# Kernel tuning notes

Measured on AMD Instinct MI355X. Metric: run time of the kernel, lower is better.

The kernel has to match this reference:

```python
import jax, jax.numpy as jnp
import numpy as np

BS, N, HX, HL, HY = 512, 128, 256, 64, 128
EPS = 1e-5  # nn.LayerNorm default


def setup_inputs() -> dict:
    key = jax.random.key(0)
    ks = jax.random.split(key, 10)

    def lin(k, fan_in, fan_out):
        return jax.random.normal(k, (fan_in, fan_out), jnp.float32) / np.float32(np.sqrt(fan_in))

    return {
        "X": jax.random.normal(ks[0], (BS, N, HX), jnp.float32),
        "E": jax.random.randint(ks[1], (BS, N, N, 2), 0, 2, jnp.int32),
        "y": jax.random.normal(ks[2], (BS, HY), jnp.float32),
        "label": jax.random.normal(ks[3], (BS, N, HL), jnp.float32),
        "node_mask": jnp.ones((BS, N), jnp.bool_),
        # GCNConv aggr_X: (HX+HL) -> HX ; GCNConv aggr_label: HL -> HL
        "Wx": lin(ks[4], HX + HL, HX), "bx": jnp.zeros((HX,), jnp.float32),
        "Wl": lin(ks[5], HL, HL), "bl": jnp.zeros((HL,), jnp.float32),
        # update_X: Linear(HX+HL+HY -> HX) + ReLU + LayerNorm
        "W1": lin(ks[6], HX + HL + HY, HX), "b1": jnp.zeros((HX,), jnp.float32),
        "g1": jnp.ones((HX,), jnp.float32), "be1": jnp.zeros((HX,), jnp.float32),
        # update_label: Linear(HL -> HL) + ReLU + LayerNorm
        "W2": lin(ks[7], HL, HL), "b2": jnp.zeros((HL,), jnp.float32),
        "g2": jnp.ones((HL,), jnp.float32), "be2": jnp.zeros((HL,), jnp.float32),
    }


def _layernorm(h, g, b):
    mu = jnp.mean(h, axis=-1, keepdims=True)
    var = jnp.mean((h - mu) ** 2, axis=-1, keepdims=True)
    return (h - mu) * jax.lax.rsqrt(var + EPS) * g + b


def _gcn_norm_adj(E, node_mask, dtype):
    # adj = E[..., 1] nonzero pattern, restricted to valid nodes.
    adj = (E[..., 1] != 0).astype(dtype)  # [bs, n, n]
    m = node_mask.astype(dtype)
    adj = adj * m[:, :, None] * m[:, None, :]
    # GCNConv default: add self-loops, symmetric normalization D^-1/2 (A+I) D^-1/2
    A = adj + jnp.eye(adj.shape[-1], dtype=dtype)[None]
    deg = jnp.sum(A, axis=-1)
    dinv = jnp.where(deg > 0, jax.lax.rsqrt(jnp.maximum(deg, 1.0)), 0.0)
    return A * dinv[:, :, None] * dinv[:, None, :]


def reference(X, E, y, label, node_mask,
              Wx, bx, Wl, bl,
              W1, b1, g1, be1,
              W2, b2, g2, be2):
    bs, n, hx = X.shape
    _, hy = y.shape
    An = _gcn_norm_adj(E, node_mask, X.dtype)  # [bs, n, n]

    # aggr_X: GCNConv on cat([X, label])
    Xl = jnp.concatenate([X, label], axis=-1)              # [bs, n, hx+hl]
    Xa = jnp.einsum('bij,bjh->bih', An, Xl @ Wx) + bx      # [bs, n, hx]
    # aggr_label: GCNConv on label
    la = jnp.einsum('bij,bjh->bih', An, label @ Wl) + bl   # [bs, n, hl]

    y_expand = jnp.broadcast_to(y[:, None, :], (bs, n, hy))
    h = jnp.concatenate([Xa, la, y_expand], axis=-1)       # [bs, n, hx+hl+hy]

    X_out = _layernorm(jax.nn.relu(h @ W1 + b1), g1, be1)  # dropout in eval = identity
    label_out = _layernorm(jax.nn.relu(la @ W2 + b2), g2, be2)
    return (X_out, label_out)
```

## Files before the change

### kernel.cpp

```cpp
#include <hip/hip_runtime.h>


typedef __attribute__((ext_vector_type(8))) short bf16x8;
typedef __attribute__((ext_vector_type(4))) float f32x4;
typedef unsigned short u16;
typedef unsigned int u32;

#define OFF_WXT 0
#define OFF_W1T 81920
#define OFF_WLT 196608
#define OFF_W2T 200704
#define WS_U16  204800

__device__ __forceinline__ u16 f2bf(float f) {
  u32 u = __float_as_uint(f);
  return (u16)((u + 0x7FFFu + ((u >> 16) & 1u)) >> 16);
}
__device__ __forceinline__ float bf2f(u16 h) {
  return __uint_as_float(((u32)h) << 16);
}
__device__ __forceinline__ u32 pk2(float x, float y) {
  return (u32)f2bf(x) | ((u32)f2bf(y) << 16);
}
__device__ __forceinline__ bf16x8 pack8(float4 a, float4 b) {
  union { bf16x8 v; u32 u[4]; } r;
  r.u[0] = pk2(a.x, a.y); r.u[1] = pk2(a.z, a.w);
  r.u[2] = pk2(b.x, b.y); r.u[3] = pk2(b.z, b.w);
  return r.v;
}

#define MFMA(a, bfr, c) __builtin_amdgcn_mfma_f32_16x16x32_bf16((a), (bfr), (c), 0, 0, 0)

__global__ __launch_bounds__(256)
void wprep_kernel(const float* __restrict__ Wx, const float* __restrict__ Wl,
                  const float* __restrict__ W1, const float* __restrict__ W2,
                  u16* __restrict__ ws) {
  int t = blockIdx.x * 256 + threadIdx.x;
  if (t >= WS_U16) return;
  float v;
  if (t < 81920) {
    int n = t / 320, k = t - n * 320;
    v = Wx[k * 256 + n];
  } else if (t < 196608) {
    int t2 = t - 81920;
    int n = t2 / 448, k = t2 - n * 448;
    v = W1[k * 256 + n];
  } else if (t < 200704) {
    int t3 = t - 196608;
    int n = t3 >> 6, k = t3 & 63;
    v = Wl[k * 64 + n];
  } else {
    int t4 = t - 200704;
    int n = t4 >> 6, k = t4 & 63;
    v = W2[k * 64 + n];
  }
  ws[t] = f2bf(v);
}

__global__ __launch_bounds__(1024, 4)
void gnn_fused(const float* __restrict__ Xg, const int* __restrict__ Eg,
               const float* __restrict__ yg, const float* __restrict__ Lb,
               const float* __restrict__ bx, const float* __restrict__ blv,
               const float* __restrict__ b1, const float* __restrict__ g1,
               const float* __restrict__ be1, const float* __restrict__ b2,
               const float* __restrict__ g2, const float* __restrict__ be2,
               const u16* __restrict__ wsW,
               float* __restrict__ Xout, float* __restrict__ Lout) {
  __shared__ u16 sA[128 * 136];
  __shared__ u16 sXWT[256 * 136];
  __shared__ u16 sLWT[64 * 136];
  __shared__ u16 sH[128 * 72];
  __shared__ u16 sXbf[128 * 72];
  __shared__ float sBX[256];
  __shared__ float sBL[64];
  __shared__ float sW1YB[256];
  __shared__ float sDinv[128];
  __shared__ float2 sRed[256];

  const int tid = threadIdx.x;
  const int w = tid >> 6;
  const int lane = tid & 63;
  const int quad = lane >> 4;
  const int l15 = lane & 15;
  const int b = blockIdx.x;

  float* sDegp = reinterpret_cast<float*>(sH);
  float* sY    = reinterpret_cast<float*>(sH) + 1024;

  bf16x8 afx[10];
  {
    const u16* wrow = wsW + OFF_WXT + (w * 16 + l15) * 320 + quad * 8;
    #pragma unroll
    for (int cc = 0; cc < 10; ++cc) afx[cc] = *reinterpret_cast<const bf16x8*>(wrow + cc * 32);
  }
  bf16x8 afl[2];
  {
    const u16* wrow = wsW + OFF_WLT + ((w & 3) * 16 + l15) * 64 + quad * 8;
    afl[0] = *reinterpret_cast<const bf16x8*>(wrow);
    afl[1] = *reinterpret_cast<const bf16x8*>(wrow + 32);
  }

  if (tid < 256) sBX[tid] = bx[tid];
  else if (tid < 320) sBL[tid - 256] = blv[tid - 256];
  else if (tid < 448) sY[tid - 320] = yg[(size_t)b * 128 + (tid - 320)];

  {
    const int i = tid >> 3;
    const int qq = tid & 7;
    const int4* Erow = reinterpret_cast<const int4*>(Eg) + (size_t)b * 8192 + i * 64 + qq * 8;
    float part = 0.f;
    #pragma unroll
    for (int cc = 0; cc < 8; ++cc) {
      int4 v = Erow[cc];
      int j = qq * 16 + cc * 2;
      float a0 = (v.y != 0) ? 1.f : 0.f;
      float a1 = (v.w != 0) ? 1.f : 0.f;
      if (j == i) a0 += 1.f;
      if (j + 1 == i) a1 += 1.f;
      part += a0 + a1;
      *reinterpret_cast<u32*>(&sA[i * 136 + j]) = pk2(a0, a1);
    }
    sDegp[i * 8 + qq] = part;
  }
  __syncthreads();

  if (tid < 128) {
    float d = 0.f;
    #pragma unroll
    for (int k = 0; k < 8; ++k) d += sDegp[tid * 8 + k];
    sDinv[tid] = (d > 0.f) ? rsqrtf(fmaxf(d, 1.f)) : 0.f;
  }
  if (tid < 256) {
    float s = b1[tid];
    const u16* rowp = wsW + OFF_W1T + tid * 448 + 320;
    #pragma unroll
    for (int kk = 0; kk < 128; kk += 8) {
      bf16x8 v = *reinterpret_cast<const bf16x8*>(rowp + kk);
      #pragma unroll
      for (int t2 = 0; t2 < 8; ++t2) s += bf2f((u16)v[t2]) * sY[kk + t2];
    }
    sW1YB[tid] = s;
  }

  f32x4 acc1[8];
  #pragma unroll
  for (int jt = 0; jt < 8; ++jt) acc1[jt] = f32x4{0.f, 0.f, 0.f, 0.f};

  for (int c = 0; c < 5; ++c) {
    __syncthreads();
    {
      int j = tid >> 3;
      int kk = (tid & 7) * 8;
      const float* src = (c < 4) ? (Xg + ((size_t)(b * 128 + j)) * 256 + c * 64 + kk)
                                 : (Lb + ((size_t)(b * 128 + j)) * 64 + kk);
      float4 v0 = *reinterpret_cast<const float4*>(src);
      float4 v1 = *reinterpret_cast<const float4*>(src + 4);
      *reinterpret_cast<bf16x8*>(&sXbf[j * 72 + kk]) = pack8(v0, v1);
    }
    __syncthreads();
    #pragma unroll
    for (int ks = 0; ks < 2; ++ks) {
      #pragma unroll
      for (int jt = 0; jt < 8; ++jt) {
        bf16x8 bfr = *reinterpret_cast<const bf16x8*>(&sXbf[(jt * 16 + l15) * 72 + ks * 32 + quad * 8]);
        acc1[jt] = MFMA(afx[c * 2 + ks], bfr, acc1[jt]);
      }
    }
  }
  f32x4 accl[2];
  accl[0] = f32x4{0.f, 0.f, 0.f, 0.f};
  accl[1] = f32x4{0.f, 0.f, 0.f, 0.f};
  {
    const int jh = w >> 2;
    #pragma unroll
    for (int ks = 0; ks < 2; ++ks) {
      #pragma unroll
      for (int jj = 0; jj < 2; ++jj) {
        int j = (jh * 2 + jj) * 16 + l15;
        bf16x8 bfr = *reinterpret_cast<const bf16x8*>(&sXbf[j * 72 + ks * 32 + quad * 8]);
        accl[jj] = MFMA(afl[ks], bfr, accl[jj]);
      }
    }
  }
  #pragma unroll
  for (int jt = 0; jt < 8; ++jt) {
    float dj = sDinv[jt * 16 + l15];
    #pragma unroll
    for (int r = 0; r < 4; ++r)
      sXWT[(w * 16 + quad * 4 + r) * 136 + jt * 16 + l15] = f2bf(acc1[jt][r] * dj);
  }
  #pragma unroll
  for (int jj = 0; jj < 2; ++jj) {
    int j = ((w >> 2) * 2 + jj) * 16 + l15;
    float dj = sDinv[j];
    #pragma unroll
    for (int r = 0; r < 4; ++r)
      sLWT[((w & 3) * 16 + quad * 4 + r) * 136 + j] = f2bf(accl[jj][r] * dj);
  }
  __syncthreads();

  const int g = w >> 1, p = w & 1;
  const int i_ = g * 16 + l15;
  const float di = sDinv[i_];

  f32x4 acc3[8];
  #pragma unroll
  for (int m = 0; m < 8; ++m) {
    float4 iv = *reinterpret_cast<const float4*>(&sW1YB[(p * 8 + m) * 16 + quad * 4]);
    acc3[m][0] = iv.x; acc3[m][1] = iv.y; acc3[m][2] = iv.z; acc3[m][3] = iv.w;
  }

  for (int c = 0; c < 5; ++c) {
    const u16* Ablk = (c < 4) ? (sXWT + (c * 64) * 136) : sLWT;
    f32x4 acc2[2];
    acc2[0] = f32x4{0.f, 0.f, 0.f, 0.f};
    acc2[1] = f32x4{0.f, 0.f, 0.f, 0.f};
    #pragma unroll
    for (int ks = 0; ks < 4; ++ks) {
      bf16x8 bfr = *reinterpret_cast<const bf16x8*>(&sA[i_ * 136 + ks * 32 + quad * 8]);
      #pragma unroll
      for (int mtl = 0; mtl < 2; ++mtl) {
        bf16x8 af = *reinterpret_cast<const bf16x8*>(Ablk + ((p * 2 + mtl) * 16 + l15) * 136 + ks * 32 + quad * 8);
        acc2[mtl] = MFMA(af, bfr, acc2[mtl]);
      }
    }
    if (c > 0) __syncthreads();
    #pragma unroll
    for (int mtl = 0; mtl < 2; ++mtl) {
      ushort4 pk;
      u16* pp = reinterpret_cast<u16*>(&pk);
      #pragma unroll
      for (int r = 0; r < 4; ++r) {
        int nloc = (p * 2 + mtl) * 16 + quad * 4 + r;
        float bias = (c < 4) ? sBX[c * 64 + nloc] : sBL[nloc];
        pp[r] = f2bf(acc2[mtl][r] * di + bias);
      }
      *reinterpret_cast<ushort4*>(&sH[i_ * 72 + (p * 2 + mtl) * 16 + quad * 4]) = pk;
    }
    __syncthreads();
    #pragma unroll
    for (int ks2 = 0; ks2 < 2; ++ks2) {
      bf16x8 bh = *reinterpret_cast<const bf16x8*>(&sH[i_ * 72 + ks2 * 32 + quad * 8]);
      #pragma unroll
      for (int m = 0; m < 8; ++m) {
        bf16x8 af = *reinterpret_cast<const bf16x8*>(wsW + OFF_W1T + ((p * 8 + m) * 16 + l15) * 448 + c * 64 + ks2 * 32 + quad * 8);
        acc3[m] = MFMA(af, bh, acc3[m]);
      }
    }
  }

  {
    float s = 0.f, s2 = 0.f;
    #pragma unroll
    for (int m = 0; m < 8; ++m) {
      #pragma unroll
      for (int r = 0; r < 4; ++r) {
        float v = fmaxf(acc3[m][r], 0.f);
        acc3[m][r] = v;
        s += v; s2 += v * v;
      }
    }
    s  += __shfl_xor(s, 16);  s  += __shfl_xor(s, 32);
    s2 += __shfl_xor(s2, 16); s2 += __shfl_xor(s2, 32);
    if (quad == 0) sRed[p * 128 + i_] = make_float2(s, s2);
    __syncthreads();
    float2 o = sRed[(1 - p) * 128 + i_];
    s += o.x; s2 += o.y;
    float mu = s * (1.f / 256.f);
    float var = s2 * (1.f / 256.f) - mu * mu;
    float rstd = rsqrtf(var + 1e-5f);
    float* op = Xout + ((size_t)(b * 128 + i_)) * 256;
    #pragma unroll
    for (int m = 0; m < 8; ++m) {
      int f0 = (p * 8 + m) * 16 + quad * 4;
      float4 gv = *reinterpret_cast<const float4*>(g1 + f0);
      float4 bv = *reinterpret_cast<const float4*>(be1 + f0);
      float4 o4;
      o4.x = (acc3[m][0] - mu) * rstd * gv.x + bv.x;
      o4.y = (acc3[m][1] - mu) * rstd * gv.y + bv.y;
      o4.z = (acc3[m][2] - mu) * rstd * gv.z + bv.z;
      o4.w = (acc3[m][3] - mu) * rstd * gv.w + bv.w;
      *reinterpret_cast<float4*>(op + f0) = o4;
    }
  }

  if (p == 0) {
    f32x4 acc4[4];
    #pragma unroll
    for (int mt2 = 0; mt2 < 4; ++mt2) acc4[mt2] = f32x4{0.f, 0.f, 0.f, 0.f};
    #pragma unroll
    for (int ks = 0; ks < 2; ++ks) {
      bf16x8 bh = *reinterpret_cast<const bf16x8*>(&sH[i_ * 72 + ks * 32 + quad * 8]);
      #pragma unroll
      for (int mt2 = 0; mt2 < 4; ++mt2) {
        bf16x8 af = *reinterpret_cast<const bf16x8*>(wsW + OFF_W2T + (mt2 * 16 + l15) * 64 + ks * 32 + quad * 8);
        acc4[mt2] = MFMA(af, bh, acc4[mt2]);
      }
    }
    float s = 0.f, s2 = 0.f;
    #pragma unroll
    for (int mt2 = 0; mt2 < 4; ++mt2) {
      float4 bias2 = *reinterpret_cast<const float4*>(b2 + mt2 * 16 + quad * 4);
      acc4[mt2][0] = fmaxf(acc4[mt2][0] + bias2.x, 0.f);
      acc4[mt2][1] = fmaxf(acc4[mt2][1] + bias2.y, 0.f);
      acc4[mt2][2] = fmaxf(acc4[mt2][2] + bias2.z, 0.f);
      acc4[mt2][3] = fmaxf(acc4[mt2][3] + bias2.w, 0.f);
      #pragma unroll
      for (int r = 0; r < 4; ++r) { s += acc4[mt2][r]; s2 += acc4[mt2][r] * acc4[mt2][r]; }
    }
    s  += __shfl_xor(s, 16);  s  += __shfl_xor(s, 32);
    s2 += __shfl_xor(s2, 16); s2 += __shfl_xor(s2, 32);
    float mu = s * (1.f / 64.f);
    float var = s2 * (1.f / 64.f) - mu * mu;
    float rstd = rsqrtf(var + 1e-5f);
    float* op = Lout + ((size_t)(b * 128 + i_)) * 64;
    #pragma unroll
    for (int mt2 = 0; mt2 < 4; ++mt2) {
      int f0 = mt2 * 16 + quad * 4;
      float4 gv = *reinterpret_cast<const float4*>(g2 + f0);
      float4 bv = *reinterpret_cast<const float4*>(be2 + f0);
      float4 o4;
      o4.x = (acc4[mt2][0] - mu) * rstd * gv.x + bv.x;
      o4.y = (acc4[mt2][1] - mu) * rstd * gv.y + bv.y;
      o4.z = (acc4[mt2][2] - mu) * rstd * gv.z + bv.z;
      o4.w = (acc4[mt2][3] - mu) * rstd * gv.w + bv.w;
      *reinterpret_cast<float4*>(op + f0) = o4;
    }
  }
}

extern "C" void kernel_launch(void* const* d_in, const int* in_sizes, int n_in,
                              void* d_out, int out_size, void* d_ws, size_t ws_size,
                              hipStream_t stream) {
  (void)in_sizes; (void)n_in; (void)out_size; (void)ws_size;
  const float* X   = (const float*)d_in[0];
  const int*   E   = (const int*)d_in[1];
  const float* y   = (const float*)d_in[2];
  const float* lb  = (const float*)d_in[3];
  const float* Wx  = (const float*)d_in[5];
  const float* bx  = (const float*)d_in[6];
  const float* Wl  = (const float*)d_in[7];
  const float* bl  = (const float*)d_in[8];
  const float* W1  = (const float*)d_in[9];
  const float* b1  = (const float*)d_in[10];
  const float* g1  = (const float*)d_in[11];
  const float* be1 = (const float*)d_in[12];
  const float* W2  = (const float*)d_in[13];
  const float* b2  = (const float*)d_in[14];
  const float* g2  = (const float*)d_in[15];
  const float* be2 = (const float*)d_in[16];
  u16* wsW = (u16*)d_ws;
  float* Xout = (float*)d_out;
  float* Lout = Xout + (size_t)512 * 128 * 256;

  wprep_kernel<<<dim3(800), dim3(256), 0, stream>>>(Wx, Wl, W1, W2, wsW);
  gnn_fused<<<dim3(512), dim3(1024), 0, stream>>>(X, E, y, lb, bx, bl, b1, g1, be1,
                                                  b2, g2, be2, wsW, Xout, Lout);
}
```

Before: 333.2 us.

## Shrink LDS by streaming XW chunks through one buffer and reloading weights per chunk

Replaces the full sXWT/sLWT staging buffers with a single 64-row chunk buffer that each wave group fills just before it is consumed, and aliases the bf16 X staging onto sH. Wx/Wl fragments are now loaded from global memory per chunk instead of held in registers for the whole kernel, and the launch bound asks for higher occupancy. The aim is to cut LDS and register use so more blocks fit per CU. In exchange it adds a barrier per chunk, keeps the projection results in registers across phases, and issues more global weight loads.

```diff
diff --git a/kernel.cpp b/kernel.cpp
--- a/kernel.cpp
+++ b/kernel.cpp
@@ -57,7 +57,7 @@
   ws[t] = f2bf(v);
 }
 
-__global__ __launch_bounds__(1024, 4)
+__global__ __launch_bounds__(1024, 8)
 void gnn_fused(const float* __restrict__ Xg, const int* __restrict__ Eg,
                const float* __restrict__ yg, const float* __restrict__ Lb,
                const float* __restrict__ bx, const float* __restrict__ blv,
@@ -67,10 +67,8 @@
                const u16* __restrict__ wsW,
                float* __restrict__ Xout, float* __restrict__ Lout) {
   __shared__ u16 sA[128 * 136];
-  __shared__ u16 sXWT[256 * 136];
-  __shared__ u16 sLWT[64 * 136];
+  __shared__ u16 sChunk[64 * 136];
   __shared__ u16 sH[128 * 72];
-  __shared__ u16 sXbf[128 * 72];
   __shared__ float sBX[256];
   __shared__ float sBL[64];
   __shared__ float sW1YB[256];
@@ -84,21 +82,9 @@
   const int l15 = lane & 15;
   const int b = blockIdx.x;
 
+  u16* sXbf = sH;
   float* sDegp = reinterpret_cast<float*>(sH);
   float* sY    = reinterpret_cast<float*>(sH) + 1024;
-
-  bf16x8 afx[10];
-  {
-    const u16* wrow = wsW + OFF_WXT + (w * 16 + l15) * 320 + quad * 8;
-    #pragma unroll
-    for (int cc = 0; cc < 10; ++cc) afx[cc] = *reinterpret_cast<const bf16x8*>(wrow + cc * 32);
-  }
-  bf16x8 afl[2];
-  {
-    const u16* wrow = wsW + OFF_WLT + ((w & 3) * 16 + l15) * 64 + quad * 8;
-    afl[0] = *reinterpret_cast<const bf16x8*>(wrow);
-    afl[1] = *reinterpret_cast<const bf16x8*>(wrow + 32);
-  }
 
   if (tid < 256) sBX[tid] = bx[tid];
   else if (tid < 320) sBL[tid - 256] = blv[tid - 256];
@@ -157,46 +143,78 @@
       float4 v1 = *reinterpret_cast<const float4*>(src + 4);
       *reinterpret_cast<bf16x8*>(&sXbf[j * 72 + kk]) = pack8(v0, v1);
     }
-    __syncthreads();
-    #pragma unroll
-    for (int ks = 0; ks < 2; ++ks) {
-      #pragma unroll
-      for (int jt = 0; jt < 8; ++jt) {
-        bf16x8 bfr = *reinterpret_cast<const bf16x8*>(&sXbf[(jt * 16 + l15) * 72 + ks * 32 + quad * 8]);
-        acc1[jt] = MFMA(afx[c * 2 + ks], bfr, acc1[jt]);
-      }
+    const u16* wr = wsW + OFF_WXT + (w * 16 + l15) * 320 + c * 64 + quad * 8;
+    bf16x8 af0 = *reinterpret_cast<const bf16x8*>(wr);
+    bf16x8 af1 = *reinterpret_cast<const bf16x8*>(wr + 32);
+    __syncthreads();
+    #pragma unroll
+    for (int jt = 0; jt < 8; ++jt) {
+      bf16x8 bfr = *reinterpret_cast<const bf16x8*>(&sXbf[(jt * 16 + l15) * 72 + quad * 8]);
+      acc1[jt] = MFMA(af0, bfr, acc1[jt]);
+    }
+    #pragma unroll
+    for (int jt = 0; jt < 8; ++jt) {
+      bf16x8 bfr = *reinterpret_cast<const bf16x8*>(&sXbf[(jt * 16 + l15) * 72 + 32 + quad * 8]);
+      acc1[jt] = MFMA(af1, bfr, acc1[jt]);
     }
   }
   f32x4 accl[2];
   accl[0] = f32x4{0.f, 0.f, 0.f, 0.f};
   accl[1] = f32x4{0.f, 0.f, 0.f, 0.f};
   {
+    const u16* wrl = wsW + OFF_WLT + ((w & 3) * 16 + l15) * 64 + quad * 8;
+    bf16x8 al0 = *reinterpret_cast<const bf16x8*>(wrl);
+    bf16x8 al1 = *reinterpret_cast<const bf16x8*>(wrl + 32);
     const int jh = w >> 2;
     #pragma unroll
-    for (int ks = 0; ks < 2; ++ks) {
-      #pragma unroll
-      for (int jj = 0; jj < 2; ++jj) {
-        int j = (jh * 2 + jj) * 16 + l15;
-        bf16x8 bfr = *reinterpret_cast<const bf16x8*>(&sXbf[j * 72 + ks * 32 + quad * 8]);
-        accl[jj] = MFMA(afl[ks], bfr, accl[jj]);
-      }
-    }
-  }
+    for (int jj = 0; jj < 2; ++jj) {
+      int j = (jh * 2 + jj) * 16 + l15;
+      bf16x8 b0 = *reinterpret_cast<const bf16x8*>(&sXbf[j * 72 + quad * 8]);
+      accl[jj] = MFMA(al0, b0, accl[jj]);
+      bf16x8 b1 = *reinterpret_cast<const bf16x8*>(&sXbf[j * 72 + 32 + quad * 8]);
+      accl[jj] = MFMA(al1, b1, accl[jj]);
+    }
+  }
+
+  u32 xpk[16];
   #pragma unroll
   for (int jt = 0; jt < 8; ++jt) {
     float dj = sDinv[jt * 16 + l15];
-    #pragma unroll
-    for (int r = 0; r < 4; ++r)
-      sXWT[(w * 16 + quad * 4 + r) * 136 + jt * 16 + l15] = f2bf(acc1[jt][r] * dj);
-  }
+    xpk[jt * 2]     = pk2(acc1[jt][0] * dj, acc1[jt][1] * dj);
+    xpk[jt * 2 + 1] = pk2(acc1[jt][2] * dj, acc1[jt][3] * dj);
+  }
+  u32 lpk[4];
   #pragma unroll
   for (int jj = 0; jj < 2; ++jj) {
-    int j = ((w >> 2) * 2 + jj) * 16 + l15;
-    float dj = sDinv[j];
-    #pragma unroll
-    for (int r = 0; r < 4; ++r)
-      sLWT[((w & 3) * 16 + quad * 4 + r) * 136 + j] = f2bf(accl[jj][r] * dj);
-  }
+    float dj = sDinv[((w >> 2) * 2 + jj) * 16 + l15];
+    lpk[jj * 2]     = pk2(accl[jj][0] * dj, accl[jj][1] * dj);
+    lpk[jj * 2 + 1] = pk2(accl[jj][2] * dj, accl[jj][3] * dj);
+  }
+
+  auto write_xchunk = [&]() {
+    const int rbase = (w & 3) * 16 + quad * 4;
+    #pragma unroll
+    for (int jt = 0; jt < 8; ++jt) {
+      int j = jt * 16 + l15;
+      sChunk[(rbase + 0) * 136 + j] = (u16)(xpk[jt * 2] & 0xffffu);
+      sChunk[(rbase + 1) * 136 + j] = (u16)(xpk[jt * 2] >> 16);
+      sChunk[(rbase + 2) * 136 + j] = (u16)(xpk[jt * 2 + 1] & 0xffffu);
+      sChunk[(rbase + 3) * 136 + j] = (u16)(xpk[jt * 2 + 1] >> 16);
+    }
+  };
+  auto write_lchunk = [&]() {
+    const int rbase = (w & 3) * 16 + quad * 4;
+    #pragma unroll
+    for (int jj = 0; jj < 2; ++jj) {
+      int j = ((w >> 2) * 2 + jj) * 16 + l15;
+      sChunk[(rbase + 0) * 136 + j] = (u16)(lpk[jj * 2] & 0xffffu);
+      sChunk[(rbase + 1) * 136 + j] = (u16)(lpk[jj * 2] >> 16);
+      sChunk[(rbase + 2) * 136 + j] = (u16)(lpk[jj * 2 + 1] & 0xffffu);
+      sChunk[(rbase + 3) * 136 + j] = (u16)(lpk[jj * 2 + 1] >> 16);
+    }
+  };
+
+  if ((w >> 2) == 0) write_xchunk();
   __syncthreads();
 
   const int g = w >> 1, p = w & 1;
@@ -211,7 +229,6 @@
   }
 
   for (int c = 0; c < 5; ++c) {
-    const u16* Ablk = (c < 4) ? (sXWT + (c * 64) * 136) : sLWT;
     f32x4 acc2[2];
     acc2[0] = f32x4{0.f, 0.f, 0.f, 0.f};
     acc2[1] = f32x4{0.f, 0.f, 0.f, 0.f};
@@ -220,11 +237,11 @@
       bf16x8 bfr = *reinterpret_cast<const bf16x8*>(&sA[i_ * 136 + ks * 32 + quad * 8]);
       #pragma unroll
       for (int mtl = 0; mtl < 2; ++mtl) {
-        bf16x8 af = *reinterpret_cast<const bf16x8*>(Ablk + ((p * 2 + mtl) * 16 + l15) * 136 + ks * 32 + quad * 8);
+        bf16x8 af = *reinterpret_cast<const bf16x8*>(&sChunk[((p * 2 + mtl) * 16 + l15) * 136 + ks * 32 + quad * 8]);
         acc2[mtl] = MFMA(af, bfr, acc2[mtl]);
       }
     }
-    if (c > 0) __syncthreads();
+    __syncthreads();
     #pragma unroll
     for (int mtl = 0; mtl < 2; ++mtl) {
       ushort4 pk;
@@ -236,6 +253,11 @@
         pp[r] = f2bf(acc2[mtl][r] * di + bias);
       }
       *reinterpret_cast<ushort4*>(&sH[i_ * 72 + (p * 2 + mtl) * 16 + quad * 4]) = pk;
+    }
+    if (c < 3) {
+      if ((w >> 2) == c + 1) write_xchunk();
+    } else if (c == 3) {
+      write_lchunk();
     }
     __syncthreads();
     #pragma unroll
```

After: 399.9 us. 20.0% more time.

## Split fused GNN kernel into prep, feature-transform and aggregate+update kernels

Applied to the files above, without the earlier changes.

Replaces the single 1024-thread-per-batch fused kernel with three launches. A prep kernel transposes weights through shared memory, precomputes the per-batch y@W1 contribution plus bias, and builds the bf16 adjacency with self-loops and dinv. A 256-thread kernel computes dinv-scaled X·Wx and label·Wl into workspace. A second kernel splits each batch into four row-groups for aggregation, the W1/W2 linears and both layernorms. This trades extra global traffic through workspace and more launches for many more, smaller blocks and better occupancy. The old fused path is kept as a fallback when the workspace is too small.

```diff
diff --git a/kernel.cpp b/kernel.cpp
--- a/kernel.cpp
+++ b/kernel.cpp
@@ -5,12 +5,17 @@
 typedef __attribute__((ext_vector_type(4))) float f32x4;
 typedef unsigned short u16;
 typedef unsigned int u32;
+typedef unsigned char u8;
 
 #define OFF_WXT 0
 #define OFF_W1T 81920
 #define OFF_WLT 196608
 #define OFF_W2T 200704
-#define WS_U16  204800
+#define OFF_WYB 204800
+#define OFF_AB  466944
+#define OFF_DINV 8855552
+#define OFF_XWT 8986624
+#define WS_NEED 59916288ull
 
 __device__ __forceinline__ u16 f2bf(float f) {
   u32 u = __float_as_uint(f);
@@ -32,29 +37,311 @@
 #define MFMA(a, bfr, c) __builtin_amdgcn_mfma_f32_16x16x32_bf16((a), (bfr), (c), 0, 0, 0)
 
 __global__ __launch_bounds__(256)
-void wprep_kernel(const float* __restrict__ Wx, const float* __restrict__ Wl,
-                  const float* __restrict__ W1, const float* __restrict__ W2,
-                  u16* __restrict__ ws) {
-  int t = blockIdx.x * 256 + threadIdx.x;
-  if (t >= WS_U16) return;
-  float v;
-  if (t < 81920) {
-    int n = t / 320, k = t - n * 320;
-    v = Wx[k * 256 + n];
-  } else if (t < 196608) {
-    int t2 = t - 81920;
-    int n = t2 / 448, k = t2 - n * 448;
-    v = W1[k * 256 + n];
-  } else if (t < 200704) {
-    int t3 = t - 196608;
-    int n = t3 >> 6, k = t3 & 63;
-    v = Wl[k * 64 + n];
+void prep_kernel(const float* __restrict__ Wx, const float* __restrict__ Wl,
+                 const float* __restrict__ W1, const float* __restrict__ W2,
+                 const float* __restrict__ b1, const float* __restrict__ yg,
+                 const int* __restrict__ Eg, u16* __restrict__ ws) {
+  __shared__ __align__(16) u8 smem[34048];
+  const int bid = blockIdx.x;
+  const int tid = threadIdx.x;
+
+  if (bid < 50) {
+    u16 (*tile)[65] = (u16(*)[65])smem;
+    const float* src; u16* dst; int R, C, kt, nt;
+    if (bid < 20)       { src = Wx; dst = ws + OFF_WXT; R = 320; C = 256; kt = bid / 4; nt = bid & 3; }
+    else if (bid < 48)  { src = W1; dst = ws + OFF_W1T; R = 448; C = 256; kt = (bid - 20) / 4; nt = (bid - 20) & 3; }
+    else if (bid == 48) { src = Wl; dst = ws + OFF_WLT; R = 64; C = 64; kt = 0; nt = 0; }
+    else                { src = W2; dst = ws + OFF_W2T; R = 64; C = 64; kt = 0; nt = 0; }
+    const int k0 = kt * 64, n0 = nt * 64;
+    const int tr = tid >> 6, tc = tid & 63;
+    #pragma unroll
+    for (int rr = 0; rr < 16; ++rr)
+      tile[rr * 4 + tr][tc] = f2bf(src[(size_t)(k0 + rr * 4 + tr) * C + n0 + tc]);
+    __syncthreads();
+    #pragma unroll
+    for (int rr = 0; rr < 16; ++rr)
+      dst[(size_t)(n0 + rr * 4 + tr) * R + k0 + tc] = tile[tc][rr * 4 + tr];
+
+  } else if (bid < 562) {
+    float* sY = (float*)smem;
+    const int b = bid - 50, f = tid;
+    if (tid < 128) sY[tid] = yg[(size_t)b * 128 + tid];
+    __syncthreads();
+    float s = b1[f];
+    const float* wcol = W1 + (size_t)320 * 256 + f;
+    #pragma unroll 8
+    for (int d = 0; d < 128; ++d)
+      s += bf2f(f2bf(wcol[(size_t)d * 256])) * sY[d];
+    ((float*)(ws + OFF_WYB))[(size_t)b * 256 + f] = s;
+
   } else {
-    int t4 = t - 200704;
-    int n = t4 >> 6, k = t4 & 63;
-    v = W2[k * 64 + n];
-  }
-  ws[t] = f2bf(v);
+    const int b = bid - 562;
+    u16* sAr = (u16*)smem;
+    const int4* E4 = (const int4*)Eg + (size_t)b * 8192;
+    #pragma unroll
+    for (int t = 0; t < 32; ++t) {
+      int fi = tid + t * 256;
+      int i = fi >> 6, j = (fi & 63) * 2;
+      int4 v = E4[fi];
+      float a0 = (v.y != 0) ? 1.f : 0.f;
+      float a1 = (v.w != 0) ? 1.f : 0.f;
+      if (j == i) a0 += 1.f;
+      if (j + 1 == i) a1 += 1.f;
+      *(u32*)&sAr[i * 132 + j] = pk2(a0, a1);
+    }
+    __syncthreads();
+    if (tid < 128) {
+      float d = 0.f;
+      const u32* row = (const u32*)&sAr[tid * 132];
+      #pragma unroll
+      for (int t = 0; t < 64; ++t) {
+        u32 u = row[t];
+        d += bf2f((u16)(u & 0xffffu)) + bf2f((u16)(u >> 16));
+      }
+      ((float*)(ws + OFF_DINV))[(size_t)b * 128 + tid] =
+          (d > 0.f) ? rsqrtf(fmaxf(d, 1.f)) : 0.f;
+    }
+    u32* dst = (u32*)(ws + OFF_AB) + (size_t)b * 8192;
+    #pragma unroll
+    for (int t = 0; t < 32; ++t) {
+      int o = tid + t * 256;
+      int row = o >> 6, c = o & 63;
+      dst[o] = *(const u32*)&sAr[row * 132 + c * 2];
+    }
+  }
+}
+
+__global__ __launch_bounds__(256)
+void a1_kernel(const float* __restrict__ Xg, const float* __restrict__ Lb,
+               const u16* __restrict__ wsW, const float* __restrict__ dinvg,
+               u16* __restrict__ XWT) {
+  __shared__ u16 sXbf[128 * 72];
+  __shared__ float sDinv[128];
+  int bid = blockIdx.x;
+  bid = (bid & 7) * 320 + (bid >> 3);
+  const int b = bid / 5, fq = bid % 5;
+  const int tid = threadIdx.x;
+  const int wv = tid >> 6, lane = tid & 63, quad = lane >> 4, l15 = lane & 15;
+
+  if (tid < 128) sDinv[tid] = dinvg[(size_t)b * 128 + tid];
+
+  f32x4 acc[8];
+  #pragma unroll
+  for (int jt = 0; jt < 8; ++jt) acc[jt] = f32x4{0.f, 0.f, 0.f, 0.f};
+
+  const int frow0 = (fq < 4 ? fq * 64 : 256) + wv * 16;
+  const u16* wbase = (fq < 4) ? (wsW + OFF_WXT + (size_t)(frow0 + l15) * 320)
+                              : (wsW + OFF_WLT + (size_t)(wv * 16 + l15) * 64);
+  const int c0 = (fq < 4) ? 0 : 4;
+
+  for (int c = c0; c < 5; ++c) {
+    __syncthreads();
+    {
+      int j = tid >> 1, kh = tid & 1;
+      const float* src = (c < 4) ? (Xg + ((size_t)(b * 128 + j)) * 256 + c * 64 + kh * 32)
+                                 : (Lb + ((size_t)(b * 128 + j)) * 64 + kh * 32);
+      #pragma unroll
+      for (int t = 0; t < 2; ++t) {
+        float4 v0 = *(const float4*)(src + t * 16);
+        float4 v1 = *(const float4*)(src + t * 16 + 4);
+        float4 v2 = *(const float4*)(src + t * 16 + 8);
+        float4 v3 = *(const float4*)(src + t * 16 + 12);
+        *(bf16x8*)&sXbf[j * 72 + kh * 32 + t * 16] = pack8(v0, v1);
+        *(bf16x8*)&sXbf[j * 72 + kh * 32 + t * 16 + 8] = pack8(v2, v3);
+      }
+    }
+    const int kc = (fq < 4) ? c * 64 : 0;
+    bf16x8 af0 = *(const bf16x8*)(wbase + kc + quad * 8);
+    bf16x8 af1 = *(const bf16x8*)(wbase + kc + 32 + quad * 8);
+    __syncthreads();
+    #pragma unroll
+    for (int jt = 0; jt < 8; ++jt)
+      acc[jt] = MFMA(af0, *(const bf16x8*)&sXbf[(jt * 16 + l15) * 72 + quad * 8], acc[jt]);
+    #pragma unroll
+    for (int jt = 0; jt < 8; ++jt)
+      acc[jt] = MFMA(af1, *(const bf16x8*)&sXbf[(jt * 16 + l15) * 72 + 32 + quad * 8], acc[jt]);
+  }
+
+  u16* orow = XWT + (size_t)b * 40960;
+  #pragma unroll
+  for (int jt = 0; jt < 8; ++jt) {
+    int j = jt * 16 + l15;
+    float dj = sDinv[j];
+    #pragma unroll
+    for (int r = 0; r < 4; ++r)
+      orow[(size_t)(frow0 + quad * 4 + r) * 128 + j] = f2bf(acc[jt][r] * dj);
+  }
+}
+
+__global__ __launch_bounds__(256)
+void a2b_kernel(const u16* __restrict__ wsW, const u16* __restrict__ Ab,
+                const float* __restrict__ dinvg, const u16* __restrict__ XWT,
+                const float* __restrict__ wyb, const float* __restrict__ bxg,
+                const float* __restrict__ blg, const float* __restrict__ g1,
+                const float* __restrict__ be1, const float* __restrict__ b2g,
+                const float* __restrict__ g2, const float* __restrict__ be2,
+                float* __restrict__ Xout, float* __restrict__ Lout) {
+  __shared__ u16 sh[32 * 328];
+  __shared__ float sBXL[320];
+  __shared__ float sDv[32];
+  __shared__ float2 sRed[4 * 32];
+  __shared__ float2 sRedL[4 * 32];
+  int bid = blockIdx.x;
+  bid = (bid & 7) * 256 + (bid >> 3);
+  const int b = bid >> 2, ig = bid & 3;
+  const int i0 = ig * 32;
+  const int tid = threadIdx.x;
+  const int wv = tid >> 6, lane = tid & 63, quad = lane >> 4, l15 = lane & 15;
+
+  if (tid < 256) sBXL[tid] = bxg[tid];
+  if (tid < 64) sBXL[256 + tid] = blg[tid];
+  if (tid < 32) sDv[tid] = dinvg[(size_t)b * 128 + i0 + tid];
+
+  const u16* xw = XWT + (size_t)b * 40960;
+  const u16* ab = Ab + (size_t)b * 16384;
+  f32x4 acc2[5][2];
+  #pragma unroll
+  for (int ft = 0; ft < 5; ++ft) {
+    acc2[ft][0] = f32x4{0.f, 0.f, 0.f, 0.f};
+    acc2[ft][1] = f32x4{0.f, 0.f, 0.f, 0.f};
+  }
+  #pragma unroll
+  for (int ks = 0; ks < 4; ++ks) {
+    bf16x8 bfr0 = *(const bf16x8*)(ab + (size_t)(i0 + l15) * 128 + ks * 32 + quad * 8);
+    bf16x8 bfr1 = *(const bf16x8*)(ab + (size_t)(i0 + 16 + l15) * 128 + ks * 32 + quad * 8);
+    #pragma unroll
+    for (int ft = 0; ft < 5; ++ft) {
+      bf16x8 af = *(const bf16x8*)(xw + (size_t)(wv * 80 + ft * 16 + l15) * 128 + ks * 32 + quad * 8);
+      acc2[ft][0] = MFMA(af, bfr0, acc2[ft][0]);
+      acc2[ft][1] = MFMA(af, bfr1, acc2[ft][1]);
+    }
+  }
+  __syncthreads();
+  #pragma unroll
+  for (int ft = 0; ft < 5; ++ft) {
+    #pragma unroll
+    for (int it = 0; it < 2; ++it) {
+      float di = sDv[it * 16 + l15];
+      ushort4 pk; u16* pp = (u16*)&pk;
+      #pragma unroll
+      for (int r = 0; r < 4; ++r) {
+        int f = wv * 80 + ft * 16 + quad * 4 + r;
+        pp[r] = f2bf(acc2[ft][it][r] * di + sBXL[f]);
+      }
+      *(ushort4*)&sh[(it * 16 + l15) * 328 + wv * 80 + ft * 16 + quad * 4] = pk;
+    }
+  }
+  __syncthreads();
+
+  f32x4 acc3[4][2];
+  #pragma unroll
+  for (int m = 0; m < 4; ++m) {
+    float4 iv = *(const float4*)(wyb + (size_t)b * 256 + wv * 64 + m * 16 + quad * 4);
+    #pragma unroll
+    for (int it = 0; it < 2; ++it) {
+      acc3[m][it][0] = iv.x; acc3[m][it][1] = iv.y;
+      acc3[m][it][2] = iv.z; acc3[m][it][3] = iv.w;
+    }
+  }
+  const u16* w1t = wsW + OFF_W1T;
+  #pragma unroll
+  for (int ks = 0; ks < 10; ++ks) {
+    bf16x8 bh0 = *(const bf16x8*)&sh[l15 * 328 + ks * 32 + quad * 8];
+    bf16x8 bh1 = *(const bf16x8*)&sh[(16 + l15) * 328 + ks * 32 + quad * 8];
+    #pragma unroll
+    for (int m = 0; m < 4; ++m) {
+      bf16x8 af = *(const bf16x8*)(w1t + (size_t)(wv * 64 + m * 16 + l15) * 448 + ks * 32 + quad * 8);
+      acc3[m][0] = MFMA(af, bh0, acc3[m][0]);
+      acc3[m][1] = MFMA(af, bh1, acc3[m][1]);
+    }
+  }
+  f32x4 acc4[2];
+  acc4[0] = f32x4{0.f, 0.f, 0.f, 0.f};
+  acc4[1] = f32x4{0.f, 0.f, 0.f, 0.f};
+  #pragma unroll
+  for (int ks = 0; ks < 2; ++ks) {
+    bf16x8 af = *(const bf16x8*)(wsW + OFF_W2T + (size_t)(wv * 16 + l15) * 64 + ks * 32 + quad * 8);
+    bf16x8 bh0 = *(const bf16x8*)&sh[l15 * 328 + 256 + ks * 32 + quad * 8];
+    bf16x8 bh1 = *(const bf16x8*)&sh[(16 + l15) * 328 + 256 + ks * 32 + quad * 8];
+    acc4[0] = MFMA(af, bh0, acc4[0]);
+    acc4[1] = MFMA(af, bh1, acc4[1]);
+  }
+
+  float xs[2] = {0.f, 0.f}, xs2[2] = {0.f, 0.f};
+  #pragma unroll
+  for (int m = 0; m < 4; ++m)
+    #pragma unroll
+    for (int it = 0; it < 2; ++it)
+      #pragma unroll
+      for (int r = 0; r < 4; ++r) {
+        float v = fmaxf(acc3[m][it][r], 0.f);
+        acc3[m][it][r] = v;
+        xs[it] += v; xs2[it] += v * v;
+      }
+  float ls[2] = {0.f, 0.f}, ls2[2] = {0.f, 0.f};
+  {
+    float4 bias2 = *(const float4*)(b2g + wv * 16 + quad * 4);
+    #pragma unroll
+    for (int it = 0; it < 2; ++it) {
+      acc4[it][0] = fmaxf(acc4[it][0] + bias2.x, 0.f);
+      acc4[it][1] = fmaxf(acc4[it][1] + bias2.y, 0.f);
+      acc4[it][2] = fmaxf(acc4[it][2] + bias2.z, 0.f);
+      acc4[it][3] = fmaxf(acc4[it][3] + bias2.w, 0.f);
+      #pragma unroll
+      for (int r = 0; r < 4; ++r) { ls[it] += acc4[it][r]; ls2[it] += acc4[it][r] * acc4[it][r]; }
+    }
+  }
+  #pragma unroll
+  for (int it = 0; it < 2; ++it) {
+    xs[it] += __shfl_xor(xs[it], 16);  xs[it] += __shfl_xor(xs[it], 32);
+    xs2[it] += __shfl_xor(xs2[it], 16); xs2[it] += __shfl_xor(xs2[it], 32);
+    ls[it] += __shfl_xor(ls[it], 16);  ls[it] += __shfl_xor(ls[it], 32);
+    ls2[it] += __shfl_xor(ls2[it], 16); ls2[it] += __shfl_xor(ls2[it], 32);
+    if (quad == 0) {
+      sRed[wv * 32 + it * 16 + l15] = make_float2(xs[it], xs2[it]);
+      sRedL[wv * 32 + it * 16 + l15] = make_float2(ls[it], ls2[it]);
+    }
+  }
+  __syncthreads();
+
+  #pragma unroll
+  for (int it = 0; it < 2; ++it) {
+    const int n = it * 16 + l15;
+    float2 t0 = sRed[n], t1 = sRed[32 + n], t2 = sRed[64 + n], t3 = sRed[96 + n];
+    float s = t0.x + t1.x + t2.x + t3.x;
+    float s2 = t0.y + t1.y + t2.y + t3.y;
+    float mu = s * (1.f / 256.f);
+    float var = s2 * (1.f / 256.f) - mu * mu;
+    float rstd = rsqrtf(var + 1e-5f);
+    float* op = Xout + ((size_t)(b * 128 + i0 + n)) * 256;
+    #pragma unroll
+    for (int m = 0; m < 4; ++m) {
+      int f0 = wv * 64 + m * 16 + quad * 4;
+      float4 gv = *(const float4*)(g1 + f0);
+      float4 bv = *(const float4*)(be1 + f0);
+      float4 o4;
+      o4.x = (acc3[m][it][0] - mu) * rstd * gv.x + bv.x;
+      o4.y = (acc3[m][it][1] - mu) * rstd * gv.y + bv.y;
+      o4.z = (acc3[m][it][2] - mu) * rstd * gv.z + bv.z;
+      o4.w = (acc3[m][it][3] - mu) * rstd * gv.w + bv.w;
+      *(float4*)(op + f0) = o4;
+    }
+    float2 u0 = sRedL[n], u1 = sRedL[32 + n], u2 = sRedL[64 + n], u3 = sRedL[96 + n];
+    float sl = u0.x + u1.x + u2.x + u3.x;
+    float sl2 = u0.y + u1.y + u2.y + u3.y;
+    float mul_ = sl * (1.f / 64.f);
+    float varl = sl2 * (1.f / 64.f) - mul_ * mul_;
+    float rstdl = rsqrtf(varl + 1e-5f);
+    int f0 = wv * 16 + quad * 4;
+    float4 gv = *(const float4*)(g2 + f0);
+    float4 bv = *(const float4*)(be2 + f0);
+    float4 o4;
+    o4.x = (acc4[it][0] - mul_) * rstdl * gv.x + bv.x;
+    o4.y = (acc4[it][1] - mul_) * rstdl * gv.y + bv.y;
+    o4.z = (acc4[it][2] - mul_) * rstdl * gv.z + bv.z;
+    o4.w = (acc4[it][3] - mul_) * rstdl * gv.w + bv.w;
+    *(float4*)(Lout + ((size_t)(b * 128 + i0 + n)) * 64 + f0) = o4;
+  }
 }
 
 __global__ __launch_bounds__(1024, 4)
@@ -332,7 +619,7 @@
 extern "C" void kernel_launch(void* const* d_in, const int* in_sizes, int n_in,
                               void* d_out, int out_size, void* d_ws, size_t ws_size,
                               hipStream_t stream) {
-  (void)in_sizes; (void)n_in; (void)out_size; (void)ws_size;
+  (void)in_sizes; (void)n_in; (void)out_size;
   const float* X   = (const float*)d_in[0];
   const int*   E   = (const int*)d_in[1];
   const float* y   = (const float*)d_in[2];
@@ -353,7 +640,19 @@
   float* Xout = (float*)d_out;
   float* Lout = Xout + (size_t)512 * 128 * 256;
 
-  wprep_kernel<<<dim3(800), dim3(256), 0, stream>>>(Wx, Wl, W1, W2, wsW);
-  gnn_fused<<<dim3(512), dim3(1024), 0, stream>>>(X, E, y, lb, bx, bl, b1, g1, be1,
-                                                  b2, g2, be2, wsW, Xout, Lout);
-}
+  if (ws_size >= WS_NEED) {
+    float* wyb  = (float*)(wsW + OFF_WYB);
+    u16*   ab   = wsW + OFF_AB;
+    float* dinv = (float*)(wsW + OFF_DINV);
+    u16*   xwt  = wsW + OFF_XWT;
+    prep_kernel<<<dim3(1074), dim3(256), 0, stream>>>(Wx, Wl, W1, W2, b1, y, E, wsW);
+    a1_kernel<<<dim3(2560), dim3(256), 0, stream>>>(X, lb, wsW, dinv, xwt);
+    a2b_kernel<<<dim3(2048), dim3(256), 0, stream>>>(wsW, ab, dinv, xwt, wyb,
+                                                     bx, bl, g1, be1, b2, g2, be2,
+                                                     Xout, Lout);
+  } else {
+    prep_kernel<<<dim3(50), dim3(256), 0, stream>>>(Wx, Wl, W1, W2, b1, y, E, wsW);
+    gnn_fused<<<dim3(512), dim3(1024), 0, stream>>>(X, E, y, lb, bx, bl, b1, g1, be1,
+                                                    b2, g2, be2, wsW, Xout, Lout);
+  }
+}
```

After: 353.3 us. 1.06x slower.
